# Kernel optimization log

Hardware: AMD Instinct MI355X
Metric: run time of the kernel (lower is better)

## Reference

```python
import jax, jax.numpy as jnp
import numpy as np

N = 50000      # nodes
E = 800000     # edges (avg degree 16)
D = 128        # embed_dim
H = 8          # nhead
HD = D // H    # head dim = 16


def setup_inputs() -> dict:
    key = jax.random.key(0)
    ks = jax.random.split(key, 6)
    s = 1.0 / np.sqrt(D)  # ~xavier scale for square matrices
    return {
        "feats": jax.random.normal(ks[0], (N, D), jnp.float32),
        "edge_index": jax.random.randint(ks[1], (E, 2), 0, N, dtype=jnp.int64),
        "Wq": jax.random.normal(ks[2], (D, D), jnp.float32) * s,
        "bq": jnp.zeros((D,), jnp.float32),
        "Wk": jax.random.normal(ks[3], (D, D), jnp.float32) * s,
        "bk": jnp.zeros((D,), jnp.float32),
        "Wv": jax.random.normal(ks[4], (D, D), jnp.float32) * s,
        "bv": jnp.zeros((D,), jnp.float32),
        "Wo": jax.random.normal(ks[5], (D, D), jnp.float32) * s,
        "bo": jnp.zeros((D,), jnp.float32),
    }


def reference(feats, edge_index, Wq, bq, Wk, bk, Wv, bv, Wo, bo):
    # Projections (nn.Linear: x @ W.T + b), split into heads: [N, H, HD]
    q = (feats @ Wq.T + bq).reshape(N, H, HD)
    k = (feats @ Wk.T + bk).reshape(N, H, HD)
    v = (feats @ Wv.T + bv).reshape(N, H, HD)

    r = edge_index[:, 0]  # source nodes
    c = edge_index[:, 1]  # destination nodes (softmax / aggregation groups)

    # Per-edge, per-head dot-product scores: [E, H]
    scores = jnp.einsum('ehd,ehd->eh', q[c], k[r]) / np.sqrt(HD)

    # Custom scatter-softmax: src_max clamped to min 0; extra exp(-src_max) in denom
    smax = jnp.maximum(jax.ops.segment_max(scores, c, num_segments=N), 0.0)  # [N, H]
    ex = jnp.exp(scores - smax[c])                                           # [E, H]
    denom = jax.ops.segment_sum(ex, c, num_segments=N)                       # [N, H]
    attn = ex / (denom + jnp.exp(-smax))[c]                                  # [E, H]

    # Weighted V per edge, scatter-mean to destination nodes
    out_e = attn[:, :, None] * v[r]                      # [E, H, HD]
    agg = jax.ops.segment_sum(out_e, c, num_segments=N)  # [N, H, HD]
    cnt = jax.ops.segment_sum(jnp.ones((E,), jnp.float32), c, num_segments=N)
    agg = agg / jnp.maximum(cnt, 1.0)[:, None, None]

    return agg.reshape(N, D) @ Wo.T + bo
```

## Files before the change

kernel.cpp:

```cpp
#include <hip/hip_runtime.h>
#include <hip/hip_bf16.h>

#define N_NODES 50000
#define N_EDGES 800000
#define DIM 128
#define NHEAD 8
#define HDIM 16
#define ELL_PAD 64
#define ELL_BLOCKS 391
#define ROWTILES 3125
#define OUT_WAVES (ROWTILES * 2)
#define OUT_GRID ((OUT_WAVES + 3) / 4)

#define Q_OFF      0ull
#define KV_OFF     12800000ull
#define AGG_OFF    38400000ull
#define ELL_OFF    51200000ull
#define CNT_OFF    64000000ull
#define WBF_OFF    64200192ull
#define BIAS_OFF   64331264ull

typedef __attribute__((ext_vector_type(8))) short short8;
typedef __attribute__((ext_vector_type(4))) float floatx4;

__device__ inline float bflo2f(unsigned u) { return __uint_as_float(u << 16); }
__device__ inline float bfhi2f(unsigned u) { return __uint_as_float(u & 0xffff0000u); }
__device__ inline unsigned short f2bf(float f) {
    unsigned u = __float_as_uint(f);
    return (unsigned short)((u + 0x7fffu + ((u >> 16) & 1u)) >> 16);
}

__device__ inline void detect_flags(const void* feats, const void* edge,
                                    int& isbf, int& is32) {
    const unsigned short* f = (const unsigned short*)feats;
    const unsigned int* eg = (const unsigned int*)edge;
    int lane = threadIdx.x & 63;
    unsigned e = (f[lane] >> 7) & 0xFF;
    int junk = (e >= 0x90 || (e > 0 && e <= 0x60)) ? 1 : 0;
    unsigned long long jm = __ballot(junk);
    int nz = (lane < 32 && eg[2 * lane + 1] != 0) ? 1 : 0;
    unsigned long long nm = __ballot(nz);
    isbf = (jm == 0ull) ? 1 : 0;
    is32 = (nm != 0ull) ? 1 : 0;
}

__device__ inline void load_edge(const int* edge, int is32, int e, int& r, int& c) {
    if (is32) { int2 p = ((const int2*)edge)[e]; r = p.x; c = p.y; }
    else {
        const long long* p = (const long long*)edge;
        r = (int)p[2 * e]; c = (int)p[2 * e + 1];
    }
    if ((unsigned)r >= N_NODES) r = 0;
    if ((unsigned)c >= N_NODES) c = 0;
}

__device__ inline float ldf(const void* p, int isbf, int i) {
    return isbf ? __bfloat162float(((const __hip_bfloat16*)p)[i])
                : ((const float*)p)[i];
}

__device__ inline short8 ldfrag(const void* base, int isbf, size_t off) {
    if (isbf) return *(const short8*)((const unsigned short*)base + off);
    const float* f = (const float*)base + off;
    float4 f0 = *(const float4*)f;
    float4 f1 = *(const float4*)(f + 4);
    short8 a;
    a[0] = (short)f2bf(f0.x); a[1] = (short)f2bf(f0.y);
    a[2] = (short)f2bf(f0.z); a[3] = (short)f2bf(f0.w);
    a[4] = (short)f2bf(f1.x); a[5] = (short)f2bf(f1.y);
    a[6] = (short)f2bf(f1.z); a[7] = (short)f2bf(f1.w);
    return a;
}

__global__ __launch_bounds__(256) void ell_build(const void* feats, const int* edge,
                                                 const void* wq, const void* wk,
                                                 const void* wv, const void* wo,
                                                 const void* bq, const void* bk,
                                                 const void* bv, const void* bo,
                                                 int* cnt, int* ell,
                                                 unsigned short* wbf, float* bias) {
    int isbf, is32; detect_flags(feats, edge, isbf, is32);

    if (blockIdx.x >= ELL_BLOCKS) {
        int b2 = blockIdx.x - ELL_BLOCKS;
        if (b2 == 256) {
            for (int j = threadIdx.x; j < 512; j += 256) {
                int m2 = j >> 7;
                const void* bb = (m2 == 0) ? bq : (m2 == 1) ? bk : (m2 == 2) ? bv : bo;
                bias[j] = ldf(bb, isbf, j & 127);
            }
            return;
        }
        if (isbf) return;
        int idx = b2 * 256 + (int)threadIdx.x;
        int mm = idx >> 14, rem = idx & 16383;
        const void* wsrc = (mm == 0) ? wq : (mm == 1) ? wk : (mm == 2) ? wv : wo;
        wbf[idx] = f2bf(((const float*)wsrc)[rem]);
        return;
    }

    int base = blockIdx.x * 2048 + (int)threadIdx.x;
    #pragma unroll
    for (int j = 0; j < 8; ++j) {
        int e = base + j * 256;
        if (e < N_EDGES) {
            int r, c; load_edge(edge, is32, e, r, c);
            int slot = atomicAdd(cnt + c, 1);
            if (slot < ELL_PAD) ell[c * ELL_PAD + slot] = r;
        }
    }
}

__global__ __launch_bounds__(192) void qkv_mfma(const void* feats_raw, const int* edge,
                                                const void* wq_raw, const void* wk_raw,
                                                const void* wv_raw,
                                                const unsigned short* wbf,
                                                const float* bias,
                                                unsigned short* q_s, unsigned short* kv_s) {
    int isbf, is32; detect_flags(feats_raw, edge, isbf, is32);
    int rowtile = blockIdx.x;
    int m = threadIdx.x >> 6;
    int lane = threadIdx.x & 63;
    int mrow = lane & 15, quad = lane >> 4;
    int arow = rowtile * 16 + mrow;

    short8 a[4];
    #pragma unroll
    for (int kt = 0; kt < 4; ++kt)
        a[kt] = ldfrag(feats_raw, isbf, (size_t)arow * DIM + quad * 8 + kt * 32);

    const void* wraw = (m == 0) ? wq_raw : (m == 1) ? wk_raw : wv_raw;
    const unsigned short* wm = isbf ? (const unsigned short*)wraw : wbf + m * 16384;
    int soff = (m == 2) ? 16 : 0;

    for (int nt = 0; nt < 8; ++nt) {
        float b = bias[m * 128 + nt * 16 + mrow];
        floatx4 acc = {b, b, b, b};
        const unsigned short* wp = wm + (size_t)(nt * 16 + mrow) * DIM + quad * 8;
        #pragma unroll
        for (int kt = 0; kt < 4; ++kt) {
            short8 bf = *(const short8*)(wp + kt * 32);
            acc = __builtin_amdgcn_mfma_f32_16x16x32_bf16(a[kt], bf, acc, 0, 0, 0);
        }
        if (m == 0) {
            #pragma unroll
            for (int r4 = 0; r4 < 4; ++r4) {
                int row = rowtile * 16 + quad * 4 + r4;
                q_s[(size_t)row * DIM + nt * 16 + mrow] = f2bf(acc[r4]);
            }
        } else {
            #pragma unroll
            for (int r4 = 0; r4 < 4; ++r4) {
                int row = rowtile * 16 + quad * 4 + r4;
                kv_s[(size_t)row * 256 + nt * 32 + soff + mrow] = f2bf(acc[r4]);
            }
        }
    }
}

__global__ __launch_bounds__(256) void node_agg(const int* __restrict__ cnt,
                                                const int* __restrict__ ell,
                                                const unsigned short* __restrict__ q_s,
                                                const uint4* __restrict__ kvpack,
                                                uint4* __restrict__ agg_bf) {
    int node = (blockIdx.x * 256 + threadIdx.x) >> 6;
    int lane = threadIdx.x & 63;
    if (node >= N_NODES) return;
    int e = lane >> 3, h = lane & 7;

    const uint4* qp = (const uint4*)(q_s + (size_t)node * DIM + h * HDIM);
    uint4 q0 = qp[0], q1 = qp[1];
    float qv[16];
    qv[0]  = bflo2f(q0.x); qv[1]  = bfhi2f(q0.x);
    qv[2]  = bflo2f(q0.y); qv[3]  = bfhi2f(q0.y);
    qv[4]  = bflo2f(q0.z); qv[5]  = bfhi2f(q0.z);
    qv[6]  = bflo2f(q0.w); qv[7]  = bfhi2f(q0.w);
    qv[8]  = bflo2f(q1.x); qv[9]  = bfhi2f(q1.x);
    qv[10] = bflo2f(q1.y); qv[11] = bfhi2f(q1.y);
    qv[12] = bflo2f(q1.z); qv[13] = bfhi2f(q1.z);
    qv[14] = bflo2f(q1.w); qv[15] = bfhi2f(q1.w);

    int degt = cnt[node];
    int deg = degt < ELL_PAD ? degt : ELL_PAD;
    float l = 0.f;
    float acc[16];
    #pragma unroll
    for (int i = 0; i < 16; ++i) acc[i] = 0.f;

    const int* erow = ell + node * ELL_PAD;
    for (int i0 = 0; i0 < deg; i0 += 16) {
        int i1 = i0 + e, i2 = i0 + 8 + e;
        bool ok1 = i1 < deg, ok2 = i2 < deg;
        int r1 = ok1 ? erow[i1] : 0;
        int r2 = ok2 ? erow[i2] : 0;
        const uint4* kp1 = kvpack + (size_t)r1 * 32 + h * 4;
        const uint4* kp2 = kvpack + (size_t)r2 * 32 + h * 4;
        uint4 ka1 = kp1[0], kb1 = kp1[1], va1 = kp1[2], vb1 = kp1[3];
        uint4 ka2 = kp2[0], kb2 = kp2[1], va2 = kp2[2], vb2 = kp2[3];

        float s1 = 0.f;
        s1 += bflo2f(ka1.x) * qv[0]  + bfhi2f(ka1.x) * qv[1];
        s1 += bflo2f(ka1.y) * qv[2]  + bfhi2f(ka1.y) * qv[3];
        s1 += bflo2f(ka1.z) * qv[4]  + bfhi2f(ka1.z) * qv[5];
        s1 += bflo2f(ka1.w) * qv[6]  + bfhi2f(ka1.w) * qv[7];
        s1 += bflo2f(kb1.x) * qv[8]  + bfhi2f(kb1.x) * qv[9];
        s1 += bflo2f(kb1.y) * qv[10] + bfhi2f(kb1.y) * qv[11];
        s1 += bflo2f(kb1.z) * qv[12] + bfhi2f(kb1.z) * qv[13];
        s1 += bflo2f(kb1.w) * qv[14] + bfhi2f(kb1.w) * qv[15];
        float p1 = ok1 ? __expf(s1 * 0.25f) : 0.f;
        l += p1;
        acc[0]  += p1 * bflo2f(va1.x); acc[1]  += p1 * bfhi2f(va1.x);
        acc[2]  += p1 * bflo2f(va1.y); acc[3]  += p1 * bfhi2f(va1.y);
        acc[4]  += p1 * bflo2f(va1.z); acc[5]  += p1 * bfhi2f(va1.z);
        acc[6]  += p1 * bflo2f(va1.w); acc[7]  += p1 * bfhi2f(va1.w);
        acc[8]  += p1 * bflo2f(vb1.x); acc[9]  += p1 * bfhi2f(vb1.x);
        acc[10] += p1 * bflo2f(vb1.y); acc[11] += p1 * bfhi2f(vb1.y);
        acc[12] += p1 * bflo2f(vb1.z); acc[13] += p1 * bfhi2f(vb1.z);
        acc[14] += p1 * bflo2f(vb1.w); acc[15] += p1 * bfhi2f(vb1.w);

        float s2 = 0.f;
        s2 += bflo2f(ka2.x) * qv[0]  + bfhi2f(ka2.x) * qv[1];
        s2 += bflo2f(ka2.y) * qv[2]  + bfhi2f(ka2.y) * qv[3];
        s2 += bflo2f(ka2.z) * qv[4]  + bfhi2f(ka2.z) * qv[5];
        s2 += bflo2f(ka2.w) * qv[6]  + bfhi2f(ka2.w) * qv[7];
        s2 += bflo2f(kb2.x) * qv[8]  + bfhi2f(kb2.x) * qv[9];
        s2 += bflo2f(kb2.y) * qv[10] + bfhi2f(kb2.y) * qv[11];
        s2 += bflo2f(kb2.z) * qv[12] + bfhi2f(kb2.z) * qv[13];
        s2 += bflo2f(kb2.w) * qv[14] + bfhi2f(kb2.w) * qv[15];
        float p2 = ok2 ? __expf(s2 * 0.25f) : 0.f;
        l += p2;
        acc[0]  += p2 * bflo2f(va2.x); acc[1]  += p2 * bfhi2f(va2.x);
        acc[2]  += p2 * bflo2f(va2.y); acc[3]  += p2 * bfhi2f(va2.y);
        acc[4]  += p2 * bflo2f(va2.z); acc[5]  += p2 * bfhi2f(va2.z);
        acc[6]  += p2 * bflo2f(va2.w); acc[7]  += p2 * bfhi2f(va2.w);
        acc[8]  += p2 * bflo2f(vb2.x); acc[9]  += p2 * bfhi2f(vb2.x);
        acc[10] += p2 * bflo2f(vb2.y); acc[11] += p2 * bfhi2f(vb2.y);
        acc[12] += p2 * bflo2f(vb2.z); acc[13] += p2 * bfhi2f(vb2.z);
        acc[14] += p2 * bflo2f(vb2.w); acc[15] += p2 * bfhi2f(vb2.w);
    }

    #pragma unroll
    for (int m = 8; m < 64; m <<= 1) {
        l += __shfl_xor(l, m);
        #pragma unroll
        for (int i = 0; i < 16; ++i) acc[i] += __shfl_xor(acc[i], m);
    }

    float inv = 1.0f / ((1.0f + l) * (float)(degt > 0 ? degt : 1));
    if (e == 0) {
        unsigned o[8];
        #pragma unroll
        for (int i = 0; i < 8; ++i)
            o[i] = (unsigned)f2bf(acc[2 * i] * inv) | ((unsigned)f2bf(acc[2 * i + 1] * inv) << 16);
        uint4* op = agg_bf + (size_t)node * 16 + h * 2;
        op[0] = make_uint4(o[0], o[1], o[2], o[3]);
        op[1] = make_uint4(o[4], o[5], o[6], o[7]);
    }
}

__global__ __launch_bounds__(256) void out_mfma(const unsigned short* agg_bf,
                                                const void* feats, const int* edge,
                                                const void* wo_raw,
                                                const unsigned short* wbf,
                                                const float* bias, void* out) {
    int isbf, is32; detect_flags(feats, edge, isbf, is32);
    const unsigned short* W = isbf ? (const unsigned short*)wo_raw : wbf + 3 * 16384;
    int w = blockIdx.x * 4 + (threadIdx.x >> 6);
    if (w >= OUT_WAVES) return;
    int rowtile = w >> 1;
    int nthalf = w & 1;
    int lane = threadIdx.x & 63;
    int mrow = lane & 15, quad = lane >> 4;
    int arow = rowtile * 16 + mrow;

    short8 a[4];
    const unsigned short* ap = agg_bf + (size_t)arow * DIM + quad * 8;
    #pragma unroll
    for (int kt = 0; kt < 4; ++kt) a[kt] = *(const short8*)(ap + kt * 32);

    for (int nt = nthalf * 4; nt < nthalf * 4 + 4; ++nt) {
        float b = bias[3 * 128 + nt * 16 + mrow];
        floatx4 acc = {b, b, b, b};
        const unsigned short* wp = W + (size_t)(nt * 16 + mrow) * DIM + quad * 8;
        #pragma unroll
        for (int kt = 0; kt < 4; ++kt) {
            short8 bf = *(const short8*)(wp + kt * 32);
            acc = __builtin_amdgcn_mfma_f32_16x16x32_bf16(a[kt], bf, acc, 0, 0, 0);
        }
        if (isbf) {
            #pragma unroll
            for (int r4 = 0; r4 < 4; ++r4) {
                int row = rowtile * 16 + quad * 4 + r4;
                ((unsigned short*)out)[(size_t)row * DIM + nt * 16 + mrow] = f2bf(acc[r4]);
            }
        } else {
            #pragma unroll
            for (int r4 = 0; r4 < 4; ++r4) {
                int row = rowtile * 16 + quad * 4 + r4;
                ((float*)out)[(size_t)row * DIM + nt * 16 + mrow] = acc[r4];
            }
        }
    }
}

extern "C" void kernel_launch(void* const* d_in, const int* in_sizes, int n_in,
                              void* d_out, int out_size, void* d_ws, size_t ws_size,
                              hipStream_t stream) {
    const void* feats = d_in[0];
    const int*  edge  = (const int*)d_in[1];
    const void* Wq = d_in[2]; const void* bq = d_in[3];
    const void* Wk = d_in[4]; const void* bk = d_in[5];
    const void* Wv = d_in[6]; const void* bv = d_in[7];
    const void* Wo = d_in[8]; const void* bo = d_in[9];

    char* ws = (char*)d_ws;
    unsigned short* q_s  = (unsigned short*)(ws + Q_OFF);
    unsigned short* kv_s = (unsigned short*)(ws + KV_OFF);
    unsigned short* aggb = (unsigned short*)(ws + AGG_OFF);
    int* ell             = (int*)(ws + ELL_OFF);
    int* cnt             = (int*)(ws + CNT_OFF);
    unsigned short* wbf  = (unsigned short*)(ws + WBF_OFF);
    float* bias          = (float*)(ws + BIAS_OFF);

    hipMemsetAsync(ws + CNT_OFF, 0, N_NODES * 4, stream);

    ell_build<<<ELL_BLOCKS + 257, 256, 0, stream>>>(feats, edge, Wq, Wk, Wv, Wo,
                                                    bq, bk, bv, bo, cnt, ell,
                                                    wbf, bias);

    qkv_mfma<<<ROWTILES, 192, 0, stream>>>(feats, edge, Wq, Wk, Wv, wbf, bias,
                                           q_s, kv_s);

    node_agg<<<(N_NODES * 64 + 255) / 256, 256, 0, stream>>>(cnt, ell, q_s,
                                                             (const uint4*)(ws + KV_OFF),
                                                             (uint4*)aggb);

    out_mfma<<<OUT_GRID, 256, 0, stream>>>(aggb, feats, edge, Wo, wbf, bias, d_out);
}
```

Before: 263.5 us.

## Fuse all stages into one persistent kernel with software grid barriers

Replaces the four separate launches (ELL build, QKV projection, node aggregation, output projection) with a single persistent kernel of 1024 blocks. ELL build and QKV projection run concurrently on disjoint block ranges, then atomic-counter grid barriers separate the aggregation and output stages. ELL insertion is partitioned by destination node modulo 8 across block groups, presumably to spread atomic contention. The bf16 weight/bias pre-conversion is dropped, so fp32 weights are converted on the fly inside each MFMA loop. The software barrier assumes all 1024 blocks are co-resident, which risks deadlock if occupancy is lower, and the per-task weight conversion adds repeated work.

```diff
diff --git a/kernel.cpp b/kernel.cpp
--- a/kernel.cpp
+++ b/kernel.cpp
@@ -7,18 +7,22 @@
 #define NHEAD 8
 #define HDIM 16
 #define ELL_PAD 64
-#define ELL_BLOCKS 391
+
+#define GRID 1024
+#define NWAVES (GRID * 4)
+#define ELL_BLKS 320
+#define EDGE_CHUNK 20000
+#define QKV_NW ((GRID - ELL_BLKS) * 4)
+#define QKV_TASKS 9375
+#define OUT_TASKS 6250
 #define ROWTILES 3125
-#define OUT_WAVES (ROWTILES * 2)
-#define OUT_GRID ((OUT_WAVES + 3) / 4)
 
 #define Q_OFF      0ull
 #define KV_OFF     12800000ull
 #define AGG_OFF    38400000ull
 #define ELL_OFF    51200000ull
 #define CNT_OFF    64000000ull
-#define WBF_OFF    64200192ull
-#define BIAS_OFF   64331264ull
+#define BAR_OFF    64200192ull
 
 typedef __attribute__((ext_vector_type(8))) short short8;
 typedef __attribute__((ext_vector_type(4))) float floatx4;
@@ -72,232 +76,219 @@
     return a;
 }
 
-__global__ __launch_bounds__(256) void ell_build(const void* feats, const int* edge,
-                                                 const void* wq, const void* wk,
-                                                 const void* wv, const void* wo,
-                                                 const void* bq, const void* bk,
-                                                 const void* bv, const void* bo,
-                                                 int* cnt, int* ell,
-                                                 unsigned short* wbf, float* bias) {
-    int isbf, is32; detect_flags(feats, edge, isbf, is32);
-
-    if (blockIdx.x >= ELL_BLOCKS) {
-        int b2 = blockIdx.x - ELL_BLOCKS;
-        if (b2 == 256) {
-            for (int j = threadIdx.x; j < 512; j += 256) {
-                int m2 = j >> 7;
-                const void* bb = (m2 == 0) ? bq : (m2 == 1) ? bk : (m2 == 2) ? bv : bo;
-                bias[j] = ldf(bb, isbf, j & 127);
-            }
-            return;
+__device__ __forceinline__ void gridbar(int* bar, int target) {
+    __syncthreads();
+    if (threadIdx.x == 0) {
+        __threadfence();
+        __hip_atomic_fetch_add(bar, 1, __ATOMIC_ACQ_REL, __HIP_MEMORY_SCOPE_AGENT);
+        while (__hip_atomic_load(bar, __ATOMIC_ACQUIRE, __HIP_MEMORY_SCOPE_AGENT) < target)
+            __builtin_amdgcn_s_sleep(8);
+        __threadfence();
+    }
+    __syncthreads();
+}
+
+__global__ __launch_bounds__(256, 4) void fused(const void* feats_raw, const int* edge,
+                                                const void* wq_raw, const void* bq,
+                                                const void* wk_raw, const void* bk,
+                                                const void* wv_raw, const void* bv,
+                                                const void* wo_raw, const void* bo,
+                                                unsigned short* q_s, unsigned short* kv_s,
+                                                unsigned short* aggb,
+                                                int* ell, int* cnt, int* bar,
+                                                void* out) {
+    int isbf, is32; detect_flags(feats_raw, edge, isbf, is32);
+    int blk = blockIdx.x;
+    int lane = threadIdx.x & 63;
+    int gw = blk * 4 + (threadIdx.x >> 6);
+
+    if (blk < ELL_BLKS) {
+        int pid = blk & 7, sub = blk >> 3;
+        int beg = sub * EDGE_CHUNK;
+        for (int e = beg + (int)threadIdx.x; e < beg + EDGE_CHUNK; e += 256) {
+            int r, c; load_edge(edge, is32, e, r, c);
+            if ((c & 7) == pid) {
+                int slot = atomicAdd(cnt + c, 1);
+                if (slot < ELL_PAD) ell[c * ELL_PAD + slot] = r;
+            }
         }
-        if (isbf) return;
-        int idx = b2 * 256 + (int)threadIdx.x;
-        int mm = idx >> 14, rem = idx & 16383;
-        const void* wsrc = (mm == 0) ? wq : (mm == 1) ? wk : (mm == 2) ? wv : wo;
-        wbf[idx] = f2bf(((const float*)wsrc)[rem]);
-        return;
-    }
-
-    int base = blockIdx.x * 2048 + (int)threadIdx.x;
-    #pragma unroll
-    for (int j = 0; j < 8; ++j) {
-        int e = base + j * 256;
-        if (e < N_EDGES) {
-            int r, c; load_edge(edge, is32, e, r, c);
-            int slot = atomicAdd(cnt + c, 1);
-            if (slot < ELL_PAD) ell[c * ELL_PAD + slot] = r;
+    } else {
+        int qw = (blk - ELL_BLKS) * 4 + (threadIdx.x >> 6);
+        int mrow = lane & 15, quad = lane >> 4;
+        for (int t = qw; t < QKV_TASKS; t += QKV_NW) {
+            int rowtile = t / 3;
+            int m = t - rowtile * 3;
+            int arow = rowtile * 16 + mrow;
+
+            short8 a[4];
+            #pragma unroll
+            for (int kt = 0; kt < 4; ++kt)
+                a[kt] = ldfrag(feats_raw, isbf, (size_t)arow * DIM + quad * 8 + kt * 32);
+
+            const void* wraw = (m == 0) ? wq_raw : (m == 1) ? wk_raw : wv_raw;
+            const void* braw = (m == 0) ? bq : (m == 1) ? bk : bv;
+            int soff = (m == 2) ? 16 : 0;
+
+            for (int nt = 0; nt < 8; ++nt) {
+                float b = ldf(braw, isbf, nt * 16 + mrow);
+                floatx4 acc = {b, b, b, b};
+                #pragma unroll
+                for (int kt = 0; kt < 4; ++kt) {
+                    short8 bf = ldfrag(wraw, isbf,
+                                       (size_t)(nt * 16 + mrow) * DIM + quad * 8 + kt * 32);
+                    acc = __builtin_amdgcn_mfma_f32_16x16x32_bf16(a[kt], bf, acc, 0, 0, 0);
+                }
+                if (m == 0) {
+                    #pragma unroll
+                    for (int r4 = 0; r4 < 4; ++r4) {
+                        int row = rowtile * 16 + quad * 4 + r4;
+                        q_s[(size_t)row * DIM + nt * 16 + mrow] = f2bf(acc[r4]);
+                    }
+                } else {
+                    #pragma unroll
+                    for (int r4 = 0; r4 < 4; ++r4) {
+                        int row = rowtile * 16 + quad * 4 + r4;
+                        kv_s[(size_t)row * 256 + nt * 32 + soff + mrow] = f2bf(acc[r4]);
+                    }
+                }
+            }
         }
     }
-}
-
-__global__ __launch_bounds__(192) void qkv_mfma(const void* feats_raw, const int* edge,
-                                                const void* wq_raw, const void* wk_raw,
-                                                const void* wv_raw,
-                                                const unsigned short* wbf,
-                                                const float* bias,
-                                                unsigned short* q_s, unsigned short* kv_s) {
-    int isbf, is32; detect_flags(feats_raw, edge, isbf, is32);
-    int rowtile = blockIdx.x;
-    int m = threadIdx.x >> 6;
-    int lane = threadIdx.x & 63;
-    int mrow = lane & 15, quad = lane >> 4;
-    int arow = rowtile * 16 + mrow;
-
-    short8 a[4];
-    #pragma unroll
-    for (int kt = 0; kt < 4; ++kt)
-        a[kt] = ldfrag(feats_raw, isbf, (size_t)arow * DIM + quad * 8 + kt * 32);
-
-    const void* wraw = (m == 0) ? wq_raw : (m == 1) ? wk_raw : wv_raw;
-    const unsigned short* wm = isbf ? (const unsigned short*)wraw : wbf + m * 16384;
-    int soff = (m == 2) ? 16 : 0;
-
-    for (int nt = 0; nt < 8; ++nt) {
-        float b = bias[m * 128 + nt * 16 + mrow];
-        floatx4 acc = {b, b, b, b};
-        const unsigned short* wp = wm + (size_t)(nt * 16 + mrow) * DIM + quad * 8;
-        #pragma unroll
-        for (int kt = 0; kt < 4; ++kt) {
-            short8 bf = *(const short8*)(wp + kt * 32);
-            acc = __builtin_amdgcn_mfma_f32_16x16x32_bf16(a[kt], bf, acc, 0, 0, 0);
+
+    gridbar(bar, GRID);
+
+    {
+        int e = lane >> 3, h = lane & 7;
+        const uint4* kvpack = (const uint4*)kv_s;
+        for (int node = gw; node < N_NODES; node += NWAVES) {
+            const uint4* qp = (const uint4*)(q_s + (size_t)node * DIM + h * HDIM);
+            uint4 q0 = qp[0], q1 = qp[1];
+            float qv[16];
+            qv[0]  = bflo2f(q0.x); qv[1]  = bfhi2f(q0.x);
+            qv[2]  = bflo2f(q0.y); qv[3]  = bfhi2f(q0.y);
+            qv[4]  = bflo2f(q0.z); qv[5]  = bfhi2f(q0.z);
+            qv[6]  = bflo2f(q0.w); qv[7]  = bfhi2f(q0.w);
+            qv[8]  = bflo2f(q1.x); qv[9]  = bfhi2f(q1.x);
+            qv[10] = bflo2f(q1.y); qv[11] = bfhi2f(q1.y);
+            qv[12] = bflo2f(q1.z); qv[13] = bfhi2f(q1.z);
+            qv[14] = bflo2f(q1.w); qv[15] = bfhi2f(q1.w);
+
+            int degt = cnt[node];
+            int deg = degt < ELL_PAD ? degt : ELL_PAD;
+            float l = 0.f;
+            float acc[16];
+            #pragma unroll
+            for (int i = 0; i < 16; ++i) acc[i] = 0.f;
+
+            const int* erow = ell + node * ELL_PAD;
+            for (int i0 = 0; i0 < deg; i0 += 16) {
+                int i1 = i0 + e, i2 = i0 + 8 + e;
+                bool ok1 = i1 < deg, ok2 = i2 < deg;
+                int r1 = ok1 ? erow[i1] : 0;
+                int r2 = ok2 ? erow[i2] : 0;
+                const uint4* kp1 = kvpack + (size_t)r1 * 32 + h * 4;
+                const uint4* kp2 = kvpack + (size_t)r2 * 32 + h * 4;
+                uint4 ka1 = kp1[0], kb1 = kp1[1], va1 = kp1[2], vb1 = kp1[3];
+                uint4 ka2 = kp2[0], kb2 = kp2[1], va2 = kp2[2], vb2 = kp2[3];
+
+                float s1 = 0.f;
+                s1 += bflo2f(ka1.x) * qv[0]  + bfhi2f(ka1.x) * qv[1];
+                s1 += bflo2f(ka1.y) * qv[2]  + bfhi2f(ka1.y) * qv[3];
+                s1 += bflo2f(ka1.z) * qv[4]  + bfhi2f(ka1.z) * qv[5];
+                s1 += bflo2f(ka1.w) * qv[6]  + bfhi2f(ka1.w) * qv[7];
+                s1 += bflo2f(kb1.x) * qv[8]  + bfhi2f(kb1.x) * qv[9];
+                s1 += bflo2f(kb1.y) * qv[10] + bfhi2f(kb1.y) * qv[11];
+                s1 += bflo2f(kb1.z) * qv[12] + bfhi2f(kb1.z) * qv[13];
+                s1 += bflo2f(kb1.w) * qv[14] + bfhi2f(kb1.w) * qv[15];
+                float p1 = ok1 ? __expf(s1 * 0.25f) : 0.f;
+                l += p1;
+                acc[0]  += p1 * bflo2f(va1.x); acc[1]  += p1 * bfhi2f(va1.x);
+                acc[2]  += p1 * bflo2f(va1.y); acc[3]  += p1 * bfhi2f(va1.y);
+                acc[4]  += p1 * bflo2f(va1.z); acc[5]  += p1 * bfhi2f(va1.z);
+                acc[6]  += p1 * bflo2f(va1.w); acc[7]  += p1 * bfhi2f(va1.w);
+                acc[8]  += p1 * bflo2f(vb1.x); acc[9]  += p1 * bfhi2f(vb1.x);
+                acc[10] += p1 * bflo2f(vb1.y); acc[11] += p1 * bfhi2f(vb1.y);
+                acc[12] += p1 * bflo2f(vb1.z); acc[13] += p1 * bfhi2f(vb1.z);
+                acc[14] += p1 * bflo2f(vb1.w); acc[15] += p1 * bfhi2f(vb1.w);
+
+                float s2 = 0.f;
+                s2 += bflo2f(ka2.x) * qv[0]  + bfhi2f(ka2.x) * qv[1];
+                s2 += bflo2f(ka2.y) * qv[2]  + bfhi2f(ka2.y) * qv[3];
+                s2 += bflo2f(ka2.z) * qv[4]  + bfhi2f(ka2.z) * qv[5];
+                s2 += bflo2f(ka2.w) * qv[6]  + bfhi2f(ka2.w) * qv[7];
+                s2 += bflo2f(kb2.x) * qv[8]  + bfhi2f(kb2.x) * qv[9];
+                s2 += bflo2f(kb2.y) * qv[10] + bfhi2f(kb2.y) * qv[11];
+                s2 += bflo2f(kb2.z) * qv[12] + bfhi2f(kb2.z) * qv[13];
+                s2 += bflo2f(kb2.w) * qv[14] + bfhi2f(kb2.w) * qv[15];
+                float p2 = ok2 ? __expf(s2 * 0.25f) : 0.f;
+                l += p2;
+                acc[0]  += p2 * bflo2f(va2.x); acc[1]  += p2 * bfhi2f(va2.x);
+                acc[2]  += p2 * bflo2f(va2.y); acc[3]  += p2 * bfhi2f(va2.y);
+                acc[4]  += p2 * bflo2f(va2.z); acc[5]  += p2 * bfhi2f(va2.z);
+                acc[6]  += p2 * bflo2f(va2.w); acc[7]  += p2 * bfhi2f(va2.w);
+                acc[8]  += p2 * bflo2f(vb2.x); acc[9]  += p2 * bfhi2f(vb2.x);
+                acc[10] += p2 * bflo2f(vb2.y); acc[11] += p2 * bfhi2f(vb2.y);
+                acc[12] += p2 * bflo2f(vb2.z); acc[13] += p2 * bfhi2f(vb2.z);
+                acc[14] += p2 * bflo2f(vb2.w); acc[15] += p2 * bfhi2f(vb2.w);
+            }
+
+            #pragma unroll
+            for (int m = 8; m < 64; m <<= 1) {
+                l += __shfl_xor(l, m);
+                #pragma unroll
+                for (int i = 0; i < 16; ++i) acc[i] += __shfl_xor(acc[i], m);
+            }
+
+            float inv = 1.0f / ((1.0f + l) * (float)(degt > 0 ? degt : 1));
+            if (e == 0) {
+                unsigned o[8];
+                #pragma unroll
+                for (int i = 0; i < 8; ++i)
+                    o[i] = (unsigned)f2bf(acc[2 * i] * inv)
+                         | ((unsigned)f2bf(acc[2 * i + 1] * inv) << 16);
+                uint4* op = (uint4*)aggb + (size_t)node * 16 + h * 2;
+                op[0] = make_uint4(o[0], o[1], o[2], o[3]);
+                op[1] = make_uint4(o[4], o[5], o[6], o[7]);
+            }
         }
-        if (m == 0) {
+    }
+
+    gridbar(bar, 2 * GRID);
+
+    {
+        int mrow = lane & 15, quad = lane >> 4;
+        for (int t = gw; t < OUT_TASKS; t += NWAVES) {
+            int rowtile = t >> 1;
+            int nthalf = t & 1;
+            int arow = rowtile * 16 + mrow;
+
+            short8 a[4];
+            const unsigned short* ap = aggb + (size_t)arow * DIM + quad * 8;
             #pragma unroll
-            for (int r4 = 0; r4 < 4; ++r4) {
-                int row = rowtile * 16 + quad * 4 + r4;
-                q_s[(size_t)row * DIM + nt * 16 + mrow] = f2bf(acc[r4]);
-            }
-        } else {
-            #pragma unroll
-            for (int r4 = 0; r4 < 4; ++r4) {
-                int row = rowtile * 16 + quad * 4 + r4;
-                kv_s[(size_t)row * 256 + nt * 32 + soff + mrow] = f2bf(acc[r4]);
-            }
-        }
-    }
-}
-
-__global__ __launch_bounds__(256) void node_agg(const int* __restrict__ cnt,
-                                                const int* __restrict__ ell,
-                                                const unsigned short* __restrict__ q_s,
-                                                const uint4* __restrict__ kvpack,
-                                                uint4* __restrict__ agg_bf) {
-    int node = (blockIdx.x * 256 + threadIdx.x) >> 6;
-    int lane = threadIdx.x & 63;
-    if (node >= N_NODES) return;
-    int e = lane >> 3, h = lane & 7;
-
-    const uint4* qp = (const uint4*)(q_s + (size_t)node * DIM + h * HDIM);
-    uint4 q0 = qp[0], q1 = qp[1];
-    float qv[16];
-    qv[0]  = bflo2f(q0.x); qv[1]  = bfhi2f(q0.x);
-    qv[2]  = bflo2f(q0.y); qv[3]  = bfhi2f(q0.y);
-    qv[4]  = bflo2f(q0.z); qv[5]  = bfhi2f(q0.z);
-    qv[6]  = bflo2f(q0.w); qv[7]  = bfhi2f(q0.w);
-    qv[8]  = bflo2f(q1.x); qv[9]  = bfhi2f(q1.x);
-    qv[10] = bflo2f(q1.y); qv[11] = bfhi2f(q1.y);
-    qv[12] = bflo2f(q1.z); qv[13] = bfhi2f(q1.z);
-    qv[14] = bflo2f(q1.w); qv[15] = bfhi2f(q1.w);
-
-    int degt = cnt[node];
-    int deg = degt < ELL_PAD ? degt : ELL_PAD;
-    float l = 0.f;
-    float acc[16];
-    #pragma unroll
-    for (int i = 0; i < 16; ++i) acc[i] = 0.f;
-
-    const int* erow = ell + node * ELL_PAD;
-    for (int i0 = 0; i0 < deg; i0 += 16) {
-        int i1 = i0 + e, i2 = i0 + 8 + e;
-        bool ok1 = i1 < deg, ok2 = i2 < deg;
-        int r1 = ok1 ? erow[i1] : 0;
-        int r2 = ok2 ? erow[i2] : 0;
-        const uint4* kp1 = kvpack + (size_t)r1 * 32 + h * 4;
-        const uint4* kp2 = kvpack + (size_t)r2 * 32 + h * 4;
-        uint4 ka1 = kp1[0], kb1 = kp1[1], va1 = kp1[2], vb1 = kp1[3];
-        uint4 ka2 = kp2[0], kb2 = kp2[1], va2 = kp2[2], vb2 = kp2[3];
-
-        float s1 = 0.f;
-        s1 += bflo2f(ka1.x) * qv[0]  + bfhi2f(ka1.x) * qv[1];
-        s1 += bflo2f(ka1.y) * qv[2]  + bfhi2f(ka1.y) * qv[3];
-        s1 += bflo2f(ka1.z) * qv[4]  + bfhi2f(ka1.z) * qv[5];
-        s1 += bflo2f(ka1.w) * qv[6]  + bfhi2f(ka1.w) * qv[7];
-        s1 += bflo2f(kb1.x) * qv[8]  + bfhi2f(kb1.x) * qv[9];
-        s1 += bflo2f(kb1.y) * qv[10] + bfhi2f(kb1.y) * qv[11];
-        s1 += bflo2f(kb1.z) * qv[12] + bfhi2f(kb1.z) * qv[13];
-        s1 += bflo2f(kb1.w) * qv[14] + bfhi2f(kb1.w) * qv[15];
-        float p1 = ok1 ? __expf(s1 * 0.25f) : 0.f;
-        l += p1;
-        acc[0]  += p1 * bflo2f(va1.x); acc[1]  += p1 * bfhi2f(va1.x);
-        acc[2]  += p1 * bflo2f(va1.y); acc[3]  += p1 * bfhi2f(va1.y);
-        acc[4]  += p1 * bflo2f(va1.z); acc[5]  += p1 * bfhi2f(va1.z);
-        acc[6]  += p1 * bflo2f(va1.w); acc[7]  += p1 * bfhi2f(va1.w);
-        acc[8]  += p1 * bflo2f(vb1.x); acc[9]  += p1 * bfhi2f(vb1.x);
-        acc[10] += p1 * bflo2f(vb1.y); acc[11] += p1 * bfhi2f(vb1.y);
-        acc[12] += p1 * bflo2f(vb1.z); acc[13] += p1 * bfhi2f(vb1.z);
-        acc[14] += p1 * bflo2f(vb1.w); acc[15] += p1 * bfhi2f(vb1.w);
-
-        float s2 = 0.f;
-        s2 += bflo2f(ka2.x) * qv[0]  + bfhi2f(ka2.x) * qv[1];
-        s2 += bflo2f(ka2.y) * qv[2]  + bfhi2f(ka2.y) * qv[3];
-        s2 += bflo2f(ka2.z) * qv[4]  + bfhi2f(ka2.z) * qv[5];
-        s2 += bflo2f(ka2.w) * qv[6]  + bfhi2f(ka2.w) * qv[7];
-        s2 += bflo2f(kb2.x) * qv[8]  + bfhi2f(kb2.x) * qv[9];
-        s2 += bflo2f(kb2.y) * qv[10] + bfhi2f(kb2.y) * qv[11];
-        s2 += bflo2f(kb2.z) * qv[12] + bfhi2f(kb2.z) * qv[13];
-        s2 += bflo2f(kb2.w) * qv[14] + bfhi2f(kb2.w) * qv[15];
-        float p2 = ok2 ? __expf(s2 * 0.25f) : 0.f;
-        l += p2;
-        acc[0]  += p2 * bflo2f(va2.x); acc[1]  += p2 * bfhi2f(va2.x);
-        acc[2]  += p2 * bflo2f(va2.y); acc[3]  += p2 * bfhi2f(va2.y);
-        acc[4]  += p2 * bflo2f(va2.z); acc[5]  += p2 * bfhi2f(va2.z);
-        acc[6]  += p2 * bflo2f(va2.w); acc[7]  += p2 * bfhi2f(va2.w);
-        acc[8]  += p2 * bflo2f(vb2.x); acc[9]  += p2 * bfhi2f(vb2.x);
-        acc[10] += p2 * bflo2f(vb2.y); acc[11] += p2 * bfhi2f(vb2.y);
-        acc[12] += p2 * bflo2f(vb2.z); acc[13] += p2 * bfhi2f(vb2.z);
-        acc[14] += p2 * bflo2f(vb2.w); acc[15] += p2 * bfhi2f(vb2.w);
-    }
-
-    #pragma unroll
-    for (int m = 8; m < 64; m <<= 1) {
-        l += __shfl_xor(l, m);
-        #pragma unroll
-        for (int i = 0; i < 16; ++i) acc[i] += __shfl_xor(acc[i], m);
-    }
-
-    float inv = 1.0f / ((1.0f + l) * (float)(degt > 0 ? degt : 1));
-    if (e == 0) {
-        unsigned o[8];
-        #pragma unroll
-        for (int i = 0; i < 8; ++i)
-            o[i] = (unsigned)f2bf(acc[2 * i] * inv) | ((unsigned)f2bf(acc[2 * i + 1] * inv) << 16);
-        uint4* op = agg_bf + (size_t)node * 16 + h * 2;
-        op[0] = make_uint4(o[0], o[1], o[2], o[3]);
-        op[1] = make_uint4(o[4], o[5], o[6], o[7]);
-    }
-}
-
-__global__ __launch_bounds__(256) void out_mfma(const unsigned short* agg_bf,
-                                                const void* feats, const int* edge,
-                                                const void* wo_raw,
-                                                const unsigned short* wbf,
-                                                const float* bias, void* out) {
-    int isbf, is32; detect_flags(feats, edge, isbf, is32);
-    const unsigned short* W = isbf ? (const unsigned short*)wo_raw : wbf + 3 * 16384;
-    int w = blockIdx.x * 4 + (threadIdx.x >> 6);
-    if (w >= OUT_WAVES) return;
-    int rowtile = w >> 1;
-    int nthalf = w & 1;
-    int lane = threadIdx.x & 63;
-    int mrow = lane & 15, quad = lane >> 4;
-    int arow = rowtile * 16 + mrow;
-
-    short8 a[4];
-    const unsigned short* ap = agg_bf + (size_t)arow * DIM + quad * 8;
-    #pragma unroll
-    for (int kt = 0; kt < 4; ++kt) a[kt] = *(const short8*)(ap + kt * 32);
-
-    for (int nt = nthalf * 4; nt < nthalf * 4 + 4; ++nt) {
-        float b = bias[3 * 128 + nt * 16 + mrow];
-        floatx4 acc = {b, b, b, b};
-        const unsigned short* wp = W + (size_t)(nt * 16 + mrow) * DIM + quad * 8;
-        #pragma unroll
-        for (int kt = 0; kt < 4; ++kt) {
-            short8 bf = *(const short8*)(wp + kt * 32);
-            acc = __builtin_amdgcn_mfma_f32_16x16x32_bf16(a[kt], bf, acc, 0, 0, 0);
-        }
-        if (isbf) {
-            #pragma unroll
-            for (int r4 = 0; r4 < 4; ++r4) {
-                int row = rowtile * 16 + quad * 4 + r4;
-                ((unsigned short*)out)[(size_t)row * DIM + nt * 16 + mrow] = f2bf(acc[r4]);
-            }
-        } else {
-            #pragma unroll
-            for (int r4 = 0; r4 < 4; ++r4) {
-                int row = rowtile * 16 + quad * 4 + r4;
-                ((float*)out)[(size_t)row * DIM + nt * 16 + mrow] = acc[r4];
+            for (int kt = 0; kt < 4; ++kt) a[kt] = *(const short8*)(ap + kt * 32);
+
+            for (int nt = nthalf * 4; nt < nthalf * 4 + 4; ++nt) {
+                float b = ldf(bo, isbf, nt * 16 + mrow);
+                floatx4 acc = {b, b, b, b};
+                #pragma unroll
+                for (int kt = 0; kt < 4; ++kt) {
+                    short8 bf = ldfrag(wo_raw, isbf,
+                                       (size_t)(nt * 16 + mrow) * DIM + quad * 8 + kt * 32);
+                    acc = __builtin_amdgcn_mfma_f32_16x16x32_bf16(a[kt], bf, acc, 0, 0, 0);
+                }
+                if (isbf) {
+                    #pragma unroll
+                    for (int r4 = 0; r4 < 4; ++r4) {
+                        int row = rowtile * 16 + quad * 4 + r4;
+                        ((unsigned short*)out)[(size_t)row * DIM + nt * 16 + mrow] = f2bf(acc[r4]);
+                    }
+                } else {
+                    #pragma unroll
+                    for (int r4 = 0; r4 < 4; ++r4) {
+                        int row = rowtile * 16 + quad * 4 + r4;
+                        ((float*)out)[(size_t)row * DIM + nt * 16 + mrow] = acc[r4];
+                    }
+                }
             }
         }
     }
@@ -319,21 +310,10 @@
     unsigned short* aggb = (unsigned short*)(ws + AGG_OFF);
     int* ell             = (int*)(ws + ELL_OFF);
     int* cnt             = (int*)(ws + CNT_OFF);
-    unsigned short* wbf  = (unsigned short*)(ws + WBF_OFF);
-    float* bias          = (float*)(ws + BIAS_OFF);
-
-    hipMemsetAsync(ws + CNT_OFF, 0, N_NODES * 4, stream);
-
-    ell_build<<<ELL_BLOCKS + 257, 256, 0, stream>>>(feats, edge, Wq, Wk, Wv, Wo,
-                                                    bq, bk, bv, bo, cnt, ell,
-                                                    wbf, bias);
-
-    qkv_mfma<<<ROWTILES, 192, 0, stream>>>(feats, edge, Wq, Wk, Wv, wbf, bias,
-                                           q_s, kv_s);
-
-    node_agg<<<(N_NODES * 64 + 255) / 256, 256, 0, stream>>>(cnt, ell, q_s,
-                                                             (const uint4*)(ws + KV_OFF),
-                                                             (uint4*)aggb);
-
-    out_mfma<<<OUT_GRID, 256, 0, stream>>>(aggb, feats, edge, Wo, wbf, bias, d_out);
-}
+    int* bar             = (int*)(ws + BAR_OFF);
+
+    hipMemsetAsync(ws + CNT_OFF, 0, 200448, stream);
+
+    fused<<<GRID, 256, 0, stream>>>(feats, edge, Wq, bq, Wk, bk, Wv, bv, Wo, bo,
+                                    q_s, kv_s, aggb, ell, cnt, bar, d_out);
+}
```

After: 750.0 us. +184.6%, slower.
